# Kernel tuning notes

Hardware: AMD Instinct MI355X
Metric: run time of the kernel (lower is better)

Reference implementation:

```python
import jax, jax.numpy as jnp
import numpy as np

V, E, HID, T = 50000, 256, 512, 12   # vocab, embed dim, lstm hidden (bi total), tagset size
START, STOP = 10, 11
L = 2048                              # sentence length
H = HID // 2                          # per-direction hidden
NEG = -10000.0


def setup_inputs():
    key = jax.random.key(0)
    ks = jax.random.split(key, 13)
    s = 0.05
    sentence = jax.random.randint(ks[0], (L,), 0, V)
    embed = jax.random.normal(ks[1], (V, E), jnp.float32) * s
    w_ih_f = jax.random.normal(ks[2], (4 * H, E), jnp.float32) * s
    w_hh_f = jax.random.normal(ks[3], (4 * H, H), jnp.float32) * s
    b_ih_f = jax.random.normal(ks[4], (4 * H,), jnp.float32) * s
    b_hh_f = jax.random.normal(ks[5], (4 * H,), jnp.float32) * s
    w_ih_b = jax.random.normal(ks[6], (4 * H, E), jnp.float32) * s
    w_hh_b = jax.random.normal(ks[7], (4 * H, H), jnp.float32) * s
    b_ih_b = jax.random.normal(ks[8], (4 * H,), jnp.float32) * s
    b_hh_b = jax.random.normal(ks[9], (4 * H,), jnp.float32) * s
    w_out = jax.random.normal(ks[10], (T, HID), jnp.float32) * s
    b_out = jax.random.normal(ks[11], (T,), jnp.float32) * s
    transitions = jax.random.normal(ks[12], (T, T), jnp.float32)
    transitions = transitions.at[START, :].set(NEG).at[:, STOP].set(NEG)
    return dict(sentence=sentence, embed=embed,
                w_ih_f=w_ih_f, w_hh_f=w_hh_f, b_ih_f=b_ih_f, b_hh_f=b_hh_f,
                w_ih_b=w_ih_b, w_hh_b=w_hh_b, b_ih_b=b_ih_b, b_hh_b=b_hh_b,
                w_out=w_out, b_out=b_out, transitions=transitions)


def _lstm_dir(x, w_ih, w_hh, b, reverse):
    # x: [L, E] -> hs: [L, H]; PyTorch gate order i, f, g, o
    xg = x @ w_ih.T + b  # [L, 4H] precomputed input contribution

    def step(carry, xg_t):
        h, c = carry
        g = xg_t + h @ w_hh.T
        i, f, gg, o = jnp.split(g, 4)
        i, f, o = jax.nn.sigmoid(i), jax.nn.sigmoid(f), jax.nn.sigmoid(o)
        c = f * c + i * jnp.tanh(gg)
        h = o * jnp.tanh(c)
        return (h, c), h

    hdim = w_hh.shape[1]
    init = (jnp.zeros((hdim,), x.dtype), jnp.zeros((hdim,), x.dtype))
    _, hs = jax.lax.scan(step, init, xg, reverse=reverse)
    return hs


def _lstm_feats(sentence, embed, w_ih_f, w_hh_f, b_ih_f, b_hh_f,
                w_ih_b, w_hh_b, b_ih_b, b_hh_b, w_out, b_out):
    x = embed[sentence]                                        # [L, E]
    hf = _lstm_dir(x, w_ih_f, w_hh_f, b_ih_f + b_hh_f, False)  # [L, H]
    hb = _lstm_dir(x, w_ih_b, w_hh_b, b_ih_b + b_hh_b, True)   # [L, H]
    h = jnp.concatenate([hf, hb], axis=-1)                     # [L, 2H]
    return h @ w_out.T + b_out                                 # [L, T]


def reference(sentence, embed, w_ih_f, w_hh_f, b_ih_f, b_hh_f,
              w_ih_b, w_hh_b, b_ih_b, b_hh_b, w_out, b_out, transitions):
    feats = _lstm_feats(sentence, embed, w_ih_f, w_hh_f, b_ih_f, b_hh_f,
                        w_ih_b, w_hh_b, b_ih_b, b_hh_b, w_out, b_out)

    # Viterbi DP vectorized over tags, scanned over time
    init_v = jnp.full((T,), NEG, feats.dtype).at[START].set(0.0)

    def vstep(v, feat):
        scores = transitions + v[None, :]        # [next_tag, prev_tag]
        bp = jnp.argmax(scores, axis=1)          # best previous tag per next tag
        v_new = jnp.max(scores, axis=1) + feat
        return v_new, bp

    v, bps = jax.lax.scan(vstep, init_v, feats)  # bps: [L, T]
    terminal = v + transitions[STOP]
    best = jnp.argmax(terminal)
    path_score = terminal[best]

    def btrack(tag, bp):
        return bp[tag], tag

    _, best_path = jax.lax.scan(btrack, best, bps, reverse=True)  # [L] tags
    return path_score, best_path
```

## Files before the change

### kernel.cpp

```cpp
#include <hip/hip_runtime.h>

#define LSEQ 2048
#define TAGS 12

typedef _Float16 half2v __attribute__((ext_vector_type(2)));
typedef unsigned long long u64;

__device__ __forceinline__ float sigm(float x){ return 1.0f/(1.0f+__expf(-x)); }
__device__ __forceinline__ float tanh_fast(float x){ return 1.0f - 2.0f/(1.0f+__expf(2.0f*x)); }
__device__ __forceinline__ half2v pack2(float a, float b){
  half2v r; r.x=(_Float16)a; r.y=(_Float16)b; return r;
}

__device__ __forceinline__ void wg_barrier(){
  asm volatile("s_waitcnt lgkmcnt(0)" ::: "memory");
  __builtin_amdgcn_s_barrier();
  __builtin_amdgcn_sched_barrier(0);
  asm volatile("" ::: "memory");
}

__device__ __forceinline__ u64 load_l2(const u64* p){
  u64 r;
  asm volatile("global_load_dwordx2 %0, %1, off sc0\n\t"
               "s_waitcnt vmcnt(0)"
               : "=v"(r) : "v"(p) : "memory");
  return r;
}
__device__ __forceinline__ void store_l2(u64* p, u64 v){
  asm volatile("global_store_dwordx2 %0, %1, off sc0"
               :: "v"(p), "v"(v) : "memory");
}

__global__ void init_kernel(u64* ex)
{
  int tid = blockIdx.x*256 + threadIdx.x;
  if (tid < 1024) ex[tid] = 0ull;
}

__global__ void xg_kernel(
    const int* sent, const float* embed,
    const float* w_ih_f, const float* b_ih_f, const float* b_hh_f,
    const float* w_ih_b, const float* b_ih_b, const float* b_hh_b,
    float* xg)
{
  __shared__ float x_sh[8][256];
  int tid = threadIdx.x;
  int t0 = blockIdx.x * 8;
  for (int i=0;i<8;++i){
    int idx = sent[t0+i];
    x_sh[i][tid] = embed[(size_t)idx*256 + tid];
  }
  __syncthreads();
  for (int ri=0; ri<8; ++ri){
    int r = ri*256 + tid;
    int d = r >> 10;
    int row = r & 1023;
    const float* wr = (d ? w_ih_b : w_ih_f) + (size_t)row*256;
    const float* bi = d ? b_ih_b : b_ih_f;
    const float* bh = d ? b_hh_b : b_hh_f;
    float acc[8];
    #pragma unroll
    for (int i=0;i<8;++i) acc[i]=0.f;
    for (int k0=0;k0<256;k0+=4){
      float4 p = *(const float4*)(wr + k0);
      #pragma unroll
      for (int i=0;i<8;++i){
        acc[i] += p.x*x_sh[i][k0] + p.y*x_sh[i][k0+1]
                + p.z*x_sh[i][k0+2] + p.w*x_sh[i][k0+3];
      }
    }
    float bias = bi[row] + bh[row];
    #pragma unroll
    for (int i=0;i<8;++i)
      xg[((size_t)d*LSEQ + (size_t)(t0+i))*1024 + row] = acc[i] + bias;
  }
}

__global__ __launch_bounds__(256,1) void lstm_rec(
    const float* __restrict__ w_hh_f, const float* __restrict__ w_hh_b,
    const float* __restrict__ xg, unsigned short* __restrict__ hstH,
    u64* __restrict__ ex)
{
  int blk = blockIdx.x;
  int d = blk & 7;
  if (d > 1) return;
  int q = blk >> 3;
  int qa = (q+1)&3, qb = (q+2)&3, qc = (q+3)&3;

  int tid = threadIdx.x;
  int g = tid >> 6, l = tid & 63;
  int row = g*256 + 64*q + l;
  const float* W = d ? w_hh_b : w_hh_f;
  const float* xgd = xg + (size_t)d*LSEQ*1024;
  unsigned short* hd = hstH + (size_t)d*LSEQ*256;
  u64* exS = ex + (size_t)d*256;
  u64* exF = ex + 512 + (size_t)d*256;

  __shared__ float gate_sh[2][256];
  __shared__ unsigned h2all[128];

  half2v w[128];
  {
    const float* p0 = W + (size_t)row*256 + 64*q;
    const float* p1 = W + (size_t)row*256 + 64*qa;
    const float* p2 = W + (size_t)row*256 + 64*qb;
    const float* p3 = W + (size_t)row*256 + 64*qc;
    #pragma unroll
    for (int k0=0;k0<16;++k0){
      float4 a = *(const float4*)(p0+4*k0);
      w[2*k0]      = pack2(a.x,a.y);  w[2*k0+1]    = pack2(a.z,a.w);
      float4 b = *(const float4*)(p1+4*k0);
      w[32+2*k0]   = pack2(b.x,b.y);  w[32+2*k0+1] = pack2(b.z,b.w);
      float4 cc= *(const float4*)(p2+4*k0);
      w[64+2*k0]   = pack2(cc.x,cc.y); w[64+2*k0+1] = pack2(cc.z,cc.w);
      float4 e = *(const float4*)(p3+4*k0);
      w[96+2*k0]   = pack2(e.x,e.y);  w[96+2*k0+1] = pack2(e.z,e.w);
    }
  }
  if (tid < 128) h2all[tid] = 0u;
  float c0 = 0.f, c1 = 0.f;
  unsigned hp = 0u;
  bool use_fast = true;

  int pollj = tid - 64;
  int pollpeer = (q + 1 + (pollj>>5)) & 3;
  int pollslot = 32*pollpeer + (pollj & 31);
  int adrA = (l < 32) ? (32*qa + l) : (32*qb + (l-32));
  int adrB = 32*qc + (l & 31);
  bool is_pub  = (tid < 32);
  bool is_poll = (tid >= 64) && (tid < 160);
  __syncthreads();

  int tf = d ? (LSEQ-1) : 0;
  float xg0 = xgd[(size_t)tf*1024 + row];

  for (int s=0;s<LSEQ;++s){
    bool p = is_poll && (s > 0);
    float a0=xg0, a1=0.f, a2=0.f, a3=0.f;
    #pragma unroll
    for (int k=0;k<32;k+=4){
      unsigned p0v = __builtin_amdgcn_readlane(hp,k);
      unsigned p1v = __builtin_amdgcn_readlane(hp,k+1);
      unsigned p2v = __builtin_amdgcn_readlane(hp,k+2);
      unsigned p3v = __builtin_amdgcn_readlane(hp,k+3);
      a0 = __builtin_amdgcn_fdot2(__builtin_bit_cast(half2v,p0v), w[k],   a0, false);
      a1 = __builtin_amdgcn_fdot2(__builtin_bit_cast(half2v,p1v), w[k+1], a1, false);
      a2 = __builtin_amdgcn_fdot2(__builtin_bit_cast(half2v,p2v), w[k+2], a2, false);
      a3 = __builtin_amdgcn_fdot2(__builtin_bit_cast(half2v,p3v), w[k+3], a3, false);
    }
    float nxg = 0.f;
    if (s+1 < LSEQ){
      int tn = d ? (LSEQ-2-s) : (s+1);
      nxg = xgd[(size_t)tn*1024 + row];
    }
    if (p){
      u64 v = 0ull;
      if (use_fast){
        const u64* fp = &exF[((s&1)<<7) + pollslot];
        int spins = 0;
        do {
          v = load_l2(fp);
        } while ((unsigned)(v>>32) != (unsigned)s && ++spins < 2048);
        if ((unsigned)(v>>32) != (unsigned)s) use_fast = false;
      }
      if (!use_fast){
        while ((unsigned)(v>>32) != (unsigned)s)
          v = __hip_atomic_load(&exS[((s&1)<<7) + pollslot],
                                __ATOMIC_RELAXED, __HIP_MEMORY_SCOPE_AGENT);
      }
      h2all[pollslot] = (unsigned)v;
    }
    wg_barrier();
    unsigned hrA = h2all[adrA];
    unsigned hrB = h2all[adrB];
    #pragma unroll
    for (int k=0;k<32;k+=2){
      unsigned pA0 = __builtin_amdgcn_readlane(hrA, k);
      unsigned pA1 = __builtin_amdgcn_readlane(hrA, k+1);
      unsigned pB0 = __builtin_amdgcn_readlane(hrA, 32+k);
      unsigned pB1 = __builtin_amdgcn_readlane(hrA, 32+k+1);
      unsigned pC0 = __builtin_amdgcn_readlane(hrB, k);
      unsigned pC1 = __builtin_amdgcn_readlane(hrB, k+1);
      a0 = __builtin_amdgcn_fdot2(__builtin_bit_cast(half2v,pA0), w[32+k],   a0, false);
      a1 = __builtin_amdgcn_fdot2(__builtin_bit_cast(half2v,pA1), w[32+k+1], a1, false);
      a2 = __builtin_amdgcn_fdot2(__builtin_bit_cast(half2v,pB0), w[64+k],   a2, false);
      a3 = __builtin_amdgcn_fdot2(__builtin_bit_cast(half2v,pB1), w[64+k+1], a3, false);
      a0 = __builtin_amdgcn_fdot2(__builtin_bit_cast(half2v,pC0), w[96+k],   a0, false);
      a1 = __builtin_amdgcn_fdot2(__builtin_bit_cast(half2v,pC1), w[96+k+1], a1, false);
    }
    float pre = (a0+a1) + (a2+a3);
    float act = (g==2) ? tanh_fast(pre) : sigm(pre);
    gate_sh[s&1][tid] = act;
    wg_barrier();
    {
      int m = l & 31;
      const float* gp = gate_sh[s&1];
      float2 gi = *(const float2*)&gp[      2*m];
      float2 gf = *(const float2*)&gp[ 64 + 2*m];
      float2 gg = *(const float2*)&gp[128 + 2*m];
      float2 go = *(const float2*)&gp[192 + 2*m];
      c0 = gf.x*c0 + gi.x*gg.x;
      c1 = gf.y*c1 + gi.y*gg.y;
      float h0 = go.x * tanh_fast(c0);
      float h1 = go.y * tanh_fast(c1);
      hp = __builtin_bit_cast(unsigned, pack2(h0,h1));
    }
    if (is_pub){
      if (s+1 < LSEQ){
        u64 pv = ((u64)(unsigned)(s+1) << 32) | (u64)hp;
        store_l2(&exF[(((s+1)&1)<<7) + 32*q + tid], pv);
        atomicExch(&exS[(((s+1)&1)<<7) + 32*q + tid], pv);
      }
      int tp = d ? (LSEQ-1-s) : s;
      *(unsigned*)&hd[(size_t)tp*256 + 64*q + 2*tid] = hp;
    }
    xg0 = nxg;
  }
}

__global__ void feats_kernel(
    const unsigned short* hstH, const float* w_out, const float* b_out,
    float* feats)
{
  __shared__ float w_sh[12*520];
  __shared__ float h_sh[16*520];
  const _Float16* hf = (const _Float16*)hstH;
  int tid=threadIdx.x;
  int t0=blockIdx.x*16;
  for (int i=tid;i<12*512;i+=256){ int tag=i>>9,k=i&511; w_sh[tag*520+k]=w_out[i]; }
  for (int i=tid;i<16*512;i+=256){
    int tt=i>>9,k=i&511;
    float v = (k<256)? (float)hf[(size_t)(t0+tt)*256+k]
                     : (float)hf[(size_t)(LSEQ+t0+tt)*256 + (k-256)];
    h_sh[tt*520+k]=v;
  }
  __syncthreads();
  if (tid<192){
    int tt=tid/12, tag=tid%12;
    const float* wr=&w_sh[tag*520];
    const float* hr=&h_sh[tt*520];
    float acc=b_out[tag];
    for (int k=0;k<512;k+=4){
      float4 a=*(const float4*)(wr+k);
      float4 b=*(const float4*)(hr+k);
      acc += a.x*b.x+a.y*b.y+a.z*b.z+a.w*b.w;
    }
    feats[(size_t)(t0+tt)*12+tag]=acc;
  }
}

__global__ void BiLSTM_CRF_14405320311361_kernel(
    const float* feats, const float* trans, float* outp)
{
  __shared__ float fsh[LSEQ*12];
  __shared__ unsigned char bps[LSEQ*12];
  __shared__ float term_sh[16];
  __shared__ int ibuf[66];
  __shared__ unsigned char fmap[64*12];
  int tid = threadIdx.x;
  for (int i=tid; i<LSEQ*12/4; i+=256)
    *(float4*)&fsh[4*i] = *(const float4*)&feats[4*i];
  __syncthreads();

  int lane = tid & 63;
  int fl = (lane<12) ? lane : 0;
  float vn = 0.f;
  if (tid < 64){
    float tr[12];
    #pragma unroll
    for (int p=0;p<12;++p) tr[p] = trans[fl*12+p];
    vn = (lane==10) ? 0.f : -10000.f;
    float fa = fsh[fl];
    float fb = fsh[12+fl];
    for (int t=0;t<LSEQ;++t){
      unsigned vu = __float_as_uint(vn);
      float best; int bp; float sc;
      best = tr[0] + __uint_as_float(__builtin_amdgcn_readlane(vu,0)); bp = 0;
      sc = tr[1]  + __uint_as_float(__builtin_amdgcn_readlane(vu,1));  if(sc>best){best=sc;bp=1;}
      sc = tr[2]  + __uint_as_float(__builtin_amdgcn_readlane(vu,2));  if(sc>best){best=sc;bp=2;}
      sc = tr[3]  + __uint_as_float(__builtin_amdgcn_readlane(vu,3));  if(sc>best){best=sc;bp=3;}
      sc = tr[4]  + __uint_as_float(__builtin_amdgcn_readlane(vu,4));  if(sc>best){best=sc;bp=4;}
      sc = tr[5]  + __uint_as_float(__builtin_amdgcn_readlane(vu,5));  if(sc>best){best=sc;bp=5;}
      sc = tr[6]  + __uint_as_float(__builtin_amdgcn_readlane(vu,6));  if(sc>best){best=sc;bp=6;}
      sc = tr[7]  + __uint_as_float(__builtin_amdgcn_readlane(vu,7));  if(sc>best){best=sc;bp=7;}
      sc = tr[8]  + __uint_as_float(__builtin_amdgcn_readlane(vu,8));  if(sc>best){best=sc;bp=8;}
      sc = tr[9]  + __uint_as_float(__builtin_amdgcn_readlane(vu,9));  if(sc>best){best=sc;bp=9;}
      sc = tr[10] + __uint_as_float(__builtin_amdgcn_readlane(vu,10)); if(sc>best){best=sc;bp=10;}
      sc = tr[11] + __uint_as_float(__builtin_amdgcn_readlane(vu,11)); if(sc>best){best=sc;bp=11;}
      vn = best + fa;
      fa = fb;
      if (t+2 < LSEQ) fb = fsh[(t+2)*12+fl];
      if (lane<12) bps[t*12+lane] = (unsigned char)bp;
    }
  }
  if (tid < 12) term_sh[tid] = vn + trans[11*12+tid];
  __syncthreads();
  if (tid == 0){
    float bs=term_sh[0]; int bt=0;
    for (int p=1;p<12;++p){ if (term_sh[p]>bs){bs=term_sh[p];bt=p;} }
    outp[0] = bs;
    ibuf[64] = bt;
  }
  __syncthreads();
  if (tid < 64){
    int b = tid;
    int f[12];
    int thi = b*32+31;
    #pragma unroll
    for (int x=0;x<12;++x) f[x] = bps[thi*12+x];
    for (int t=thi-1; t>=b*32; --t){
      int base = t*12;
      #pragma unroll
      for (int x=0;x<12;++x) f[x] = bps[base + f[x]];
    }
    #pragma unroll
    for (int x=0;x<12;++x) fmap[b*12+x] = (unsigned char)f[x];
  }
  __syncthreads();
  if (tid == 0){
    int tag = ibuf[64];
    for (int b=63;b>=0;--b){ ibuf[b]=tag; tag = fmap[b*12+tag]; }
  }
  __syncthreads();
  if (tid < 64){
    int b = tid;
    int tag = ibuf[b];
    for (int t=b*32+31; t>=b*32; --t){
      outp[1+t] = (float)tag;
      tag = bps[t*12+tag];
    }
  }
}

extern "C" void kernel_launch(void* const* d_in, const int* in_sizes, int n_in,
                              void* d_out, int out_size, void* d_ws, size_t ws_size,
                              hipStream_t stream) {
  const int*   sent   = (const int*)d_in[0];
  const float* embed  = (const float*)d_in[1];
  const float* w_ih_f = (const float*)d_in[2];
  const float* w_hh_f = (const float*)d_in[3];
  const float* b_ih_f = (const float*)d_in[4];
  const float* b_hh_f = (const float*)d_in[5];
  const float* w_ih_b = (const float*)d_in[6];
  const float* w_hh_b = (const float*)d_in[7];
  const float* b_ih_b = (const float*)d_in[8];
  const float* b_hh_b = (const float*)d_in[9];
  const float* w_out  = (const float*)d_in[10];
  const float* b_out  = (const float*)d_in[11];
  const float* trans  = (const float*)d_in[12];

  float* xg = (float*)d_ws;
  unsigned short* hstH = (unsigned short*)(xg + (size_t)2*LSEQ*1024);
  u64* ex = (u64*)(hstH + (size_t)2*LSEQ*256);
  float* feats = (float*)(ex + 1024);
  float* outp  = (float*)d_out;

  init_kernel<<<dim3(4), dim3(256), 0, stream>>>(ex);
  xg_kernel<<<dim3(LSEQ/8), dim3(256), 0, stream>>>(
      sent, embed, w_ih_f, b_ih_f, b_hh_f, w_ih_b, b_ih_b, b_hh_b, xg);
  lstm_rec<<<dim3(32), dim3(256), 0, stream>>>(w_hh_f, w_hh_b, xg, hstH, ex);
  feats_kernel<<<dim3(LSEQ/16), dim3(256), 0, stream>>>(hstH, w_out, b_out, feats);
  BiLSTM_CRF_14405320311361_kernel<<<dim3(1), dim3(256), 0, stream>>>(feats, trans, outp);
}
```

Measured before the change: 3.633 ms.

## Use 128-slot ring for fast-path handoff with single cold probe and atomic fallback

Replaces the two-slot sc0-spinning fast exchange with a 128-deep ring buffer. Each poller does one plain (non-sc0) load of a slot that has not been cached recently, and falls back to atomic spinning on the slow buffer if the tag does not match. The poll is also moved ahead of the next xg prefetch. The aim is to cut per-step cross-block latency in the recurrent LSTM by avoiding stale cache hits and repeated L2 spins. In exchange it uses a larger exchange buffer that must be zeroed, and non-sc0 loads could return stale data once the ring wraps; the tag check guards against that.

```diff
diff --git a/kernel.cpp b/kernel.cpp
--- a/kernel.cpp
+++ b/kernel.cpp
@@ -2,6 +2,7 @@
 
 #define LSEQ 2048
 #define TAGS 12
+#define NSLOT 128
 
 typedef _Float16 half2v __attribute__((ext_vector_type(2)));
 typedef unsigned long long u64;
@@ -19,14 +20,14 @@
   asm volatile("" ::: "memory");
 }
 
-__device__ __forceinline__ u64 load_l2(const u64* p){
+__device__ __forceinline__ u64 probe_cold(const u64* p){
   u64 r;
-  asm volatile("global_load_dwordx2 %0, %1, off sc0\n\t"
+  asm volatile("global_load_dwordx2 %0, %1, off\n\t"
                "s_waitcnt vmcnt(0)"
                : "=v"(r) : "v"(p) : "memory");
   return r;
 }
-__device__ __forceinline__ void store_l2(u64* p, u64 v){
+__device__ __forceinline__ void store_pub(u64* p, u64 v){
   asm volatile("global_store_dwordx2 %0, %1, off sc0"
                :: "v"(p), "v"(v) : "memory");
 }
@@ -34,7 +35,7 @@
 __global__ void init_kernel(u64* ex)
 {
   int tid = blockIdx.x*256 + threadIdx.x;
-  if (tid < 1024) ex[tid] = 0ull;
+  if (tid < 1024 + NSLOT*256) ex[tid] = 0ull;
 }
 
 __global__ void xg_kernel(
@@ -94,7 +95,7 @@
   const float* xgd = xg + (size_t)d*LSEQ*1024;
   unsigned short* hd = hstH + (size_t)d*LSEQ*256;
   u64* exS = ex + (size_t)d*256;
-  u64* exF = ex + 512 + (size_t)d*256;
+  u64* exFd = ex + 1024 + (size_t)d*128;
 
   __shared__ float gate_sh[2][256];
   __shared__ unsigned h2all[128];
@@ -120,7 +121,6 @@
   if (tid < 128) h2all[tid] = 0u;
   float c0 = 0.f, c1 = 0.f;
   unsigned hp = 0u;
-  bool use_fast = true;
 
   int pollj = tid - 64;
   int pollpeer = (q + 1 + (pollj>>5)) & 3;
@@ -148,27 +148,20 @@
       a2 = __builtin_amdgcn_fdot2(__builtin_bit_cast(half2v,p2v), w[k+2], a2, false);
       a3 = __builtin_amdgcn_fdot2(__builtin_bit_cast(half2v,p3v), w[k+3], a3, false);
     }
+    if (p){
+      u64 v = probe_cold(&exFd[(((unsigned)s & (NSLOT-1))<<8) + pollslot]);
+      if ((unsigned)(v>>32) != (unsigned)s){
+        do {
+          v = __hip_atomic_load(&exS[((s&1)<<7) + pollslot],
+                                __ATOMIC_RELAXED, __HIP_MEMORY_SCOPE_AGENT);
+        } while ((unsigned)(v>>32) != (unsigned)s);
+      }
+      h2all[pollslot] = (unsigned)v;
+    }
     float nxg = 0.f;
     if (s+1 < LSEQ){
       int tn = d ? (LSEQ-2-s) : (s+1);
       nxg = xgd[(size_t)tn*1024 + row];
-    }
-    if (p){
-      u64 v = 0ull;
-      if (use_fast){
-        const u64* fp = &exF[((s&1)<<7) + pollslot];
-        int spins = 0;
-        do {
-          v = load_l2(fp);
-        } while ((unsigned)(v>>32) != (unsigned)s && ++spins < 2048);
-        if ((unsigned)(v>>32) != (unsigned)s) use_fast = false;
-      }
-      if (!use_fast){
-        while ((unsigned)(v>>32) != (unsigned)s)
-          v = __hip_atomic_load(&exS[((s&1)<<7) + pollslot],
-                                __ATOMIC_RELAXED, __HIP_MEMORY_SCOPE_AGENT);
-      }
-      h2all[pollslot] = (unsigned)v;
     }
     wg_barrier();
     unsigned hrA = h2all[adrA];
@@ -208,7 +201,7 @@
     if (is_pub){
       if (s+1 < LSEQ){
         u64 pv = ((u64)(unsigned)(s+1) << 32) | (u64)hp;
-        store_l2(&exF[(((s+1)&1)<<7) + 32*q + tid], pv);
+        store_pub(&exFd[(((unsigned)(s+1) & (NSLOT-1))<<8) + 32*q + tid], pv);
         atomicExch(&exS[(((s+1)&1)<<7) + 32*q + tid], pv);
       }
       int tp = d ? (LSEQ-1-s) : s;
@@ -352,10 +345,10 @@
   float* xg = (float*)d_ws;
   unsigned short* hstH = (unsigned short*)(xg + (size_t)2*LSEQ*1024);
   u64* ex = (u64*)(hstH + (size_t)2*LSEQ*256);
-  float* feats = (float*)(ex + 1024);
+  float* feats = (float*)(ex + 1024 + NSLOT*256);
   float* outp  = (float*)d_out;
 
-  init_kernel<<<dim3(4), dim3(256), 0, stream>>>(ex);
+  init_kernel<<<dim3((1024 + NSLOT*256)/256), dim3(256), 0, stream>>>(ex);
   xg_kernel<<<dim3(LSEQ/8), dim3(256), 0, stream>>>(
       sent, embed, w_ih_f, b_ih_f, b_hh_f, w_ih_b, b_ih_b, b_hh_b, xg);
   lstm_rec<<<dim3(32), dim3(256), 0, stream>>>(w_hh_f, w_hh_b, xg, hstH, ex);
```

Result: faster. 3.515 ms (-3.2%).

## Assign LSTM roles by XCC id and prefetch ring-buffered exchange slots

Applied to the files above, without the earlier changes.

Each block reads its XCC id and publishes it to a table. Blocks then elect four co-located blocks per direction, so the per-step hidden-state exchange stays within one XCC's L2 instead of relying on the blockIdx striding assumption. The fast exchange buffer becomes a 128-slot ring, which removes reuse hazards, and the first poll load is issued before the dot-product work so its latency overlaps compute. The cost is a startup handshake among all 32 blocks, and the code depends on enough blocks landing on one XCC; if none qualify, a direction's blocks exit.

```diff
diff --git a/kernel.cpp b/kernel.cpp
--- a/kernel.cpp
+++ b/kernel.cpp
@@ -2,6 +2,8 @@
 
 #define LSEQ 2048
 #define TAGS 12
+#define NSLOT 128
+#define NBLK 32
 
 typedef _Float16 half2v __attribute__((ext_vector_type(2)));
 typedef unsigned long long u64;
@@ -19,14 +21,7 @@
   asm volatile("" ::: "memory");
 }
 
-__device__ __forceinline__ u64 load_l2(const u64* p){
-  u64 r;
-  asm volatile("global_load_dwordx2 %0, %1, off sc0\n\t"
-               "s_waitcnt vmcnt(0)"
-               : "=v"(r) : "v"(p) : "memory");
-  return r;
-}
-__device__ __forceinline__ void store_l2(u64* p, u64 v){
+__device__ __forceinline__ void store_pub(u64* p, u64 v){
   asm volatile("global_store_dwordx2 %0, %1, off sc0"
                :: "v"(p), "v"(v) : "memory");
 }
@@ -34,7 +29,7 @@
 __global__ void init_kernel(u64* ex)
 {
   int tid = blockIdx.x*256 + threadIdx.x;
-  if (tid < 1024) ex[tid] = 0ull;
+  if (tid < 1024 + NSLOT*256 + NBLK) ex[tid] = 0ull;
 }
 
 __global__ void xg_kernel(
@@ -82,19 +77,56 @@
     u64* __restrict__ ex)
 {
   int blk = blockIdx.x;
-  int d = blk & 7;
-  if (d > 1) return;
-  int q = blk >> 3;
+  int tid = threadIdx.x;
+  u64* rtab = ex + 1024 + NSLOT*256;
+
+  __shared__ int role_sh[2];
+  if (tid == 0){
+    unsigned xcc;
+    asm volatile("s_getreg_b32 %0, hwreg(HW_REG_XCC_ID)" : "=s"(xcc));
+    xcc &= 15u;
+    atomicExch(&rtab[blk], 0x100ull | (u64)xcc);
+    unsigned xs[NBLK];
+    for (int i=0;i<NBLK;++i){
+      u64 v;
+      do {
+        v = __hip_atomic_load(&rtab[i], __ATOMIC_RELAXED, __HIP_MEMORY_SCOPE_AGENT);
+      } while (!(v & 0x100ull));
+      xs[i] = (unsigned)v & 15u;
+    }
+    int dd = -1, qq = -1;
+    unsigned taken = 0u;
+    for (int dir = 0; dir < 2; ++dir){
+      int pick = -1;
+      for (int x = 0; x < 16 && pick < 0; ++x){
+        int cnt = 0;
+        for (int i=0;i<NBLK;++i)
+          if (!((taken>>i)&1u) && xs[i]==(unsigned)x) ++cnt;
+        if (cnt >= 4) pick = x;
+      }
+      int rank = 0;
+      for (int i=0;i<NBLK && rank<4;++i){
+        if (!((taken>>i)&1u) && pick >= 0 && xs[i]==(unsigned)pick){
+          if (i == blk){ dd = dir; qq = rank; }
+          taken |= 1u<<i; ++rank;
+        }
+      }
+    }
+    role_sh[0] = dd; role_sh[1] = qq;
+  }
+  __syncthreads();
+  int d = role_sh[0];
+  int q = role_sh[1];
+  if (d < 0) return;
+
   int qa = (q+1)&3, qb = (q+2)&3, qc = (q+3)&3;
-
-  int tid = threadIdx.x;
   int g = tid >> 6, l = tid & 63;
   int row = g*256 + 64*q + l;
   const float* W = d ? w_hh_b : w_hh_f;
   const float* xgd = xg + (size_t)d*LSEQ*1024;
   unsigned short* hd = hstH + (size_t)d*LSEQ*256;
   u64* exS = ex + (size_t)d*256;
-  u64* exF = ex + 512 + (size_t)d*256;
+  u64* exFd = ex + 1024 + (size_t)d*128;
 
   __shared__ float gate_sh[2][256];
   __shared__ unsigned h2all[128];
@@ -136,6 +168,17 @@
 
   for (int s=0;s<LSEQ;++s){
     bool p = is_poll && (s > 0);
+    u64 pv_ = 0ull;
+    u64* fp = &exFd[(((unsigned)s & (NSLOT-1))<<8) + pollslot];
+    if (p && use_fast){
+      asm volatile("global_load_dwordx2 %0, %1, off sc0"
+                   : "+v"(pv_) : "v"(fp) : "memory");
+    }
+    float nxg = 0.f;
+    if (s+1 < LSEQ){
+      int tn = d ? (LSEQ-2-s) : (s+1);
+      nxg = xgd[(size_t)tn*1024 + row];
+    }
     float a0=xg0, a1=0.f, a2=0.f, a3=0.f;
     #pragma unroll
     for (int k=0;k<32;k+=4){
@@ -148,19 +191,18 @@
       a2 = __builtin_amdgcn_fdot2(__builtin_bit_cast(half2v,p2v), w[k+2], a2, false);
       a3 = __builtin_amdgcn_fdot2(__builtin_bit_cast(half2v,p3v), w[k+3], a3, false);
     }
-    float nxg = 0.f;
-    if (s+1 < LSEQ){
-      int tn = d ? (LSEQ-2-s) : (s+1);
-      nxg = xgd[(size_t)tn*1024 + row];
-    }
     if (p){
       u64 v = 0ull;
       if (use_fast){
-        const u64* fp = &exF[((s&1)<<7) + pollslot];
+        asm volatile("s_waitcnt vmcnt(1)" : "+v"(pv_) :: "memory");
+        v = pv_;
         int spins = 0;
-        do {
-          v = load_l2(fp);
-        } while ((unsigned)(v>>32) != (unsigned)s && ++spins < 2048);
+        while ((unsigned)(v>>32) != (unsigned)s && spins < 512){
+          asm volatile("global_load_dwordx2 %0, %1, off sc0\n\t"
+                       "s_waitcnt vmcnt(0)"
+                       : "+v"(v) : "v"(fp) : "memory");
+          ++spins;
+        }
         if ((unsigned)(v>>32) != (unsigned)s) use_fast = false;
       }
       if (!use_fast){
@@ -208,7 +250,7 @@
     if (is_pub){
       if (s+1 < LSEQ){
         u64 pv = ((u64)(unsigned)(s+1) << 32) | (u64)hp;
-        store_l2(&exF[(((s+1)&1)<<7) + 32*q + tid], pv);
+        store_pub(&exFd[(((unsigned)(s+1) & (NSLOT-1))<<8) + 32*q + tid], pv);
         atomicExch(&exS[(((s+1)&1)<<7) + 32*q + tid], pv);
       }
       int tp = d ? (LSEQ-1-s) : s;
@@ -352,13 +394,13 @@
   float* xg = (float*)d_ws;
   unsigned short* hstH = (unsigned short*)(xg + (size_t)2*LSEQ*1024);
   u64* ex = (u64*)(hstH + (size_t)2*LSEQ*256);
-  float* feats = (float*)(ex + 1024);
+  float* feats = (float*)(ex + 1024 + NSLOT*256 + NBLK);
   float* outp  = (float*)d_out;
 
-  init_kernel<<<dim3(4), dim3(256), 0, stream>>>(ex);
+  init_kernel<<<dim3((1024 + NSLOT*256 + NBLK + 255)/256), dim3(256), 0, stream>>>(ex);
   xg_kernel<<<dim3(LSEQ/8), dim3(256), 0, stream>>>(
       sent, embed, w_ih_f, b_ih_f, b_hh_f, w_ih_b, b_ih_b, b_hh_b, xg);
-  lstm_rec<<<dim3(32), dim3(256), 0, stream>>>(w_hh_f, w_hh_b, xg, hstH, ex);
+  lstm_rec<<<dim3(NBLK), dim3(256), 0, stream>>>(w_hh_f, w_hh_b, xg, hstH, ex);
   feats_kernel<<<dim3(LSEQ/16), dim3(256), 0, stream>>>(hstH, w_out, b_out, feats);
   BiLSTM_CRF_14405320311361_kernel<<<dim3(1), dim3(256), 0, stream>>>(feats, trans, outp);
 }
```

After: 3.423 ms. 5.8% less time.
